# Kernel optimization log

Hardware: AMD Instinct MI355X
Metric: run time of the kernel (lower is better)

Reference implementation:

```python
import jax, jax.numpy as jnp
import numpy as np
import math

B, C_IN, N_SEL, N_DROP, HEADS = 4, 128, 1024, 1024, 4
Q_OUT = K_OUT = V_OUT = 256
N = N_SEL + N_DROP


def setup_inputs() -> dict:
    key = jax.random.key(0)
    ks = jax.random.split(key, 8)
    pcd_up = jax.random.normal(ks[0], (B, C_IN, N), jnp.float32)
    points_select = jax.random.normal(ks[1], (B, C_IN, N_SEL), jnp.float32)
    points_drop = jax.random.normal(ks[2], (B, C_IN, N_DROP), jnp.float32)
    # per-batch permutation of [0, N) split into select/drop halves (collision-free scatter)
    perms = jax.vmap(lambda k: jax.random.permutation(k, N))(jax.random.split(ks[3], B))
    idx_select = perms[:, None, :N_SEL].astype(jnp.int32)
    idx_drop = perms[:, None, N_SEL:].astype(jnp.int32)
    scale = 1.0 / math.sqrt(C_IN)
    Wq = jax.random.normal(ks[4], (Q_OUT, C_IN), jnp.float32) * scale
    Wk = jax.random.normal(ks[5], (K_OUT, C_IN), jnp.float32) * scale
    Wv = jax.random.normal(ks[6], (V_OUT, C_IN), jnp.float32) * scale
    Wskip = jax.random.normal(ks[7], (V_OUT, C_IN), jnp.float32) * scale
    return {"pcd_up": pcd_up, "points_select": points_select, "points_drop": points_drop,
            "idx_select": idx_select, "idx_drop": idx_drop,
            "Wq": Wq, "Wk": Wk, "Wv": Wv, "Wskip": Wskip}


def _concat_by_idx(a, b, idx_a, idx_b):
    # scatter columns of concat([a,b]) to positions given by concat([idx_a, idx_b])
    src = jnp.concatenate([a, b], axis=-1)            # (B, C, N)
    idx = jnp.concatenate([idx_a, idx_b], axis=-1)[:, 0, :]  # (B, N)
    return jax.vmap(lambda s, i: jnp.zeros_like(s).at[:, i].set(s))(src, idx)


def reference(pcd_up, points_select, points_drop, idx_select, idx_drop, Wq, Wk, Wv, Wskip):
    b, _, n = pcd_up.shape
    x = _concat_by_idx(points_select, points_drop, idx_select, idx_drop)  # (B, C_in, N)
    # 1x1 convs (no bias) == channel matmuls, then split heads: (B, H, D, N)
    q = jnp.einsum('oc,bcn->bon', Wq, x).reshape(b, HEADS, Q_OUT // HEADS, n)
    k = jnp.einsum('oc,bcn->bon', Wk, x).reshape(b, HEADS, K_OUT // HEADS, n)
    v = jnp.einsum('oc,bcn->bon', Wv, x).reshape(b, HEADS, V_OUT // HEADS, n)
    energy = jnp.einsum('bhdn,bhdm->bhnm', q, k)      # (B, H, N, N)
    attn = jax.nn.softmax(energy / math.sqrt(Q_OUT // HEADS), axis=-1)
    out = jnp.einsum('bhnm,bhdm->bhnd', attn, v)      # (B, H, N, Dv)
    out = out.transpose(0, 2, 1, 3).reshape(b, n, V_OUT).transpose(0, 2, 1)  # (B, V_out, N)
    skip = jnp.einsum('oc,bcn->bon', Wskip, pcd_up)   # (B, V_out, N)
    return skip + out
```

## Files before the change

kernel.cpp:

```cpp
#include <hip/hip_runtime.h>
#include <hip/hip_bf16.h>
#include <math.h>

#define B_    4
#define C_IN_ 128
#define N_    2048
#define NSEL_ 1024
#define H_    4
#define KS_   2

typedef __bf16 bf16;
typedef __bf16 bf16x2 __attribute__((ext_vector_type(2)));
typedef __bf16 bf16x4 __attribute__((ext_vector_type(4)));
typedef __bf16 bf16x8 __attribute__((ext_vector_type(8)));
typedef float  f32x4  __attribute__((ext_vector_type(4)));

__device__ __forceinline__ void gll16(const void* g, void* l) {
    __builtin_amdgcn_global_load_lds((const __attribute__((address_space(1))) void*)g,
                                     (__attribute__((address_space(3))) void*)l,
                                     16, 0, 0);
}

__device__ __forceinline__ bf16x8 cvt8(float4 a, float4 b) {
    bf16x8 r;
    r[0] = (bf16)a.x; r[1] = (bf16)a.y; r[2] = (bf16)a.z; r[3] = (bf16)a.w;
    r[4] = (bf16)b.x; r[5] = (bf16)b.y; r[6] = (bf16)b.z; r[7] = (bf16)b.w;
    return r;
}

__device__ __forceinline__ float fast_exp2(float x) {
#if __has_builtin(__builtin_amdgcn_exp2f)
    return __builtin_amdgcn_exp2f(x);
#else
    return exp2f(x);
#endif
}

#define XSTR 136

__global__ __launch_bounds__(256) void qkv_mfma_kernel(
    const float* __restrict__ sel, const float* __restrict__ drop,
    const float* __restrict__ Wq, const float* __restrict__ Wk,
    const float* __restrict__ Wv,
    const int* __restrict__ isel, const int* __restrict__ idrp,
    int* __restrict__ inv,
    bf16* __restrict__ qT, bf16* __restrict__ kTt, bf16* __restrict__ vTt)
{
    const int ntile = blockIdx.x;
    const int which = blockIdx.y >> 1;
    const int rh    = blockIdx.y & 1;
    const int b     = blockIdx.z;
    const int tid   = threadIdx.x;
    const int w     = tid >> 6;
    const int lane  = tid & 63;
    const int quad  = lane >> 4;
    const int lc    = lane & 15;
    const int n0    = ntile * 64;

    __shared__ __align__(16) bf16 xT[64 * XSTR];

    if (blockIdx.y == 0 && ntile < 8) {
        int j = ntile * 256 + tid;
        int pos = (j < NSEL_) ? isel[b * NSEL_ + j] : idrp[b * NSEL_ + (j - NSEL_)];
        inv[b * N_ + (pos & (N_ - 1))] = j;
    }

    const float* srcp; int rstride;
    if (ntile < 16) { srcp = sel  + (size_t)b * C_IN_ * NSEL_ + n0;           rstride = NSEL_; }
    else            { srcp = drop + (size_t)b * C_IN_ * NSEL_ + (n0 - NSEL_); rstride = NSEL_; }

    #pragma unroll
    for (int k = 0; k < 4; ++k) {
        int e  = tid + k * 256;
        int cp = e >> 4, nq = e & 15;
        int c0 = cp * 2;
        float4 v0 = *(const float4*)(srcp + (size_t)c0 * rstride + nq * 4);
        float4 v1 = *(const float4*)(srcp + (size_t)(c0 + 1) * rstride + nq * 4);
        int cc = c0 ^ ((nq & 3) << 3);
        float a0[4] = {v0.x, v0.y, v0.z, v0.w};
        float a1[4] = {v1.x, v1.y, v1.z, v1.w};
        #pragma unroll
        for (int i = 0; i < 4; ++i) {
            int n = nq * 4 + i;
            bf16x2 t; t[0] = (bf16)a0[i]; t[1] = (bf16)a1[i];
            *(bf16x2*)&xT[n * XSTR + cc] = t;
        }
    }
    __syncthreads();

    const float* Wx = (which == 0) ? Wq : (which == 1) ? Wk : Wv;
    const int rbase = rh * 128 + w * 32;

    f32x4 acc[8];
    #pragma unroll
    for (int i = 0; i < 8; ++i) acc[i] = (f32x4){0.f, 0.f, 0.f, 0.f};

    #pragma unroll
    for (int kq = 0; kq < 4; ++kq) {
        bf16x8 wf[2], xA[4];
        #pragma unroll
        for (int ot = 0; ot < 2; ++ot) {
            const float* wp = Wx + (size_t)(rbase + ot * 16 + lc) * 128 + kq * 32 + quad * 8;
            float4 u0 = *(const float4*)wp;
            float4 u1 = *(const float4*)(wp + 4);
            wf[ot] = cvt8(u0, u1);
        }
        #pragma unroll
        for (int nt = 0; nt < 4; ++nt) {
            int row = nt * 16 + lc;
            int col = (kq * 32 + quad * 8) ^ (((row >> 2) & 3) << 3);
            xA[nt] = *(const bf16x8*)&xT[row * XSTR + col];
        }
        if (which <= 1) {
            #pragma unroll
            for (int nt = 0; nt < 4; ++nt)
                #pragma unroll
                for (int ot = 0; ot < 2; ++ot)
                    acc[nt * 2 + ot] = __builtin_amdgcn_mfma_f32_16x16x32_bf16(xA[nt], wf[ot], acc[nt * 2 + ot], 0, 0, 0);
        } else {
            #pragma unroll
            for (int ot = 0; ot < 2; ++ot)
                #pragma unroll
                for (int nt = 0; nt < 4; ++nt)
                    acc[ot * 4 + nt] = __builtin_amdgcn_mfma_f32_16x16x32_bf16(wf[ot], xA[nt], acc[ot * 4 + nt], 0, 0, 0);
        }
    }

    if (which <= 1) {
        #pragma unroll
        for (int nt = 0; nt < 4; ++nt) {
            #pragma unroll
            for (int ot = 0; ot < 2; ++ot) {
                #pragma unroll
                for (int r = 0; r < 4; ++r) {
                    int n    = n0 + nt * 16 + quad * 4 + r;
                    int rloc = nt * 16 + quad * 4 + r;
                    int o256 = rbase + ot * 16 + lc;
                    int h = o256 >> 6, d = o256 & 63;
                    float val = acc[nt * 2 + ot][r];
                    if (which == 0)
                        qT[((size_t)(b * H_ + h) * N_ + n) * 64 + d] = (bf16)(val * 0.18033688011f);
                    else
                        kTt[(((size_t)(b * H_ + h) * 32 + ntile) << 12) | (rloc << 6) | (d ^ ((rloc & 7) << 3))] = (bf16)val;
                }
            }
        }
    } else {
        #pragma unroll
        for (int ot = 0; ot < 2; ++ot) {
            #pragma unroll
            for (int r = 0; r < 4; ++r) {
                int o256 = rbase + ot * 16 + quad * 4 + r;
                int h = o256 >> 6, dv = o256 & 63;
                bf16x4 pk;
                #pragma unroll
                for (int nt = 0; nt < 4; ++nt) pk[nt] = (bf16)acc[ot * 4 + nt][r];
                int scol = (lc * 4) ^ ((dv & 7) << 3);
                *(bf16x4*)(vTt + ((((size_t)(b * H_ + h) * 32 + ntile) << 12) | (dv << 6) | scol)) = pk;
            }
        }
    }
}

#define PSTR 72

__global__ __launch_bounds__(256, 2) void attn_kernel(
    const bf16* __restrict__ qT, const bf16* __restrict__ kTt,
    const bf16* __restrict__ vTt, bf16* __restrict__ Opart,
    float* __restrict__ S_ws)
{
    const int id    = blockIdx.x;
    const int bh    = (id & 7) + 8 * ((id >> 3) & 1);
    const int qb    = (id >> 4) & 15;
    const int c     = id >> 8;
    const int b     = bh >> 2;
    const int h     = bh & 3;
    const int tid   = threadIdx.x;
    const int w     = tid >> 6;
    const int lane  = tid & 63;
    const int quad  = lane >> 4;
    const int lc    = lane & 15;
    const int n0    = qb * 128 + w * 32;

    __shared__ __align__(16) bf16 sK[2][64 * 64];
    __shared__ __align__(16) bf16 sV[2][64 * 64];
    __shared__ __align__(16) bf16 p_lds[4 * 16 * PSTR];
    bf16* pw = &p_lds[w * 16 * PSTR];

    const bf16* kbase = kTt + (((size_t)bh * 32 + c * 16) << 12);
    const bf16* vbase = vTt + (((size_t)bh * 32 + c * 16) << 12);

    #pragma unroll
    for (int j = 0; j < 2; ++j) {
        const int sseg = (w * 2 + j) << 9;
        gll16(kbase + sseg + lane * 8, &sK[0][sseg]);
        gll16(vbase + sseg + lane * 8, &sV[0][sseg]);
    }

    bf16x8 aq[2][2];
    #pragma unroll
    for (int t = 0; t < 2; ++t) {
        const bf16* qp = qT + ((size_t)bh * N_ + n0 + t * 16 + lc) * 64 + quad * 8;
        aq[t][0] = *(const bf16x8*)(qp);
        aq[t][1] = *(const bf16x8*)(qp + 32);
    }

    f32x4 accO[2][4];
    #pragma unroll
    for (int t = 0; t < 2; ++t)
        #pragma unroll
        for (int i = 0; i < 4; ++i) accO[t][i] = (f32x4){0.f, 0.f, 0.f, 0.f};
    float psum[2][4] = {{0.f,0.f,0.f,0.f},{0.f,0.f,0.f,0.f}};

    const int rswz = (lc & 7) << 3;

    for (int s = 0; s < 16; ++s) {
        const int buf = s & 1;
        __syncthreads();

        if (s < 15) {
            const bf16* kg = kbase + ((size_t)(s + 1) << 12);
            const bf16* vg = vbase + ((size_t)(s + 1) << 12);
            #pragma unroll
            for (int j = 0; j < 2; ++j) {
                const int sseg = (w * 2 + j) << 9;
                gll16(kg + sseg + lane * 8, &sK[buf ^ 1][sseg]);
                gll16(vg + sseg + lane * 8, &sV[buf ^ 1][sseg]);
            }
        }

        bf16x8 kf[4][2], vf[4][2];
        #pragma unroll
        for (int mt = 0; mt < 4; ++mt) {
            const int rb = (mt * 16 + lc) * 64;
            kf[mt][0] = *(const bf16x8*)&sK[buf][rb + ((quad * 8) ^ rswz)];
            kf[mt][1] = *(const bf16x8*)&sK[buf][rb + ((quad * 8 + 32) ^ rswz)];
            vf[mt][0] = *(const bf16x8*)&sV[buf][rb + ((quad * 8) ^ rswz)];
            vf[mt][1] = *(const bf16x8*)&sV[buf][rb + ((quad * 8 + 32) ^ rswz)];
        }

        #pragma unroll
        for (int t = 0; t < 2; ++t) {
            f32x4 accS[4];
            #pragma unroll
            for (int mt = 0; mt < 4; ++mt) {
                f32x4 z = (f32x4){0.f, 0.f, 0.f, 0.f};
                z = __builtin_amdgcn_mfma_f32_16x16x32_bf16(aq[t][0], kf[mt][0], z, 0, 0, 0);
                z = __builtin_amdgcn_mfma_f32_16x16x32_bf16(aq[t][1], kf[mt][1], z, 0, 0, 0);
                accS[mt] = z;
            }
            #pragma unroll
            for (int r = 0; r < 4; ++r) {
                float sum = 0.f;
                #pragma unroll
                for (int mt = 0; mt < 4; ++mt) {
                    float p = fast_exp2(accS[mt][r]);
                    accS[mt][r] = p;
                    sum += p;
                }
                psum[t][r] += sum;
            }
            #pragma unroll
            for (int r = 0; r < 4; ++r) {
                bf16x4 pk;
                #pragma unroll
                for (int mt = 0; mt < 4; ++mt) pk[mt] = (bf16)accS[mt][r];
                *(bf16x4*)&pw[(quad * 4 + r) * PSTR + lc * 4] = pk;
            }
            bf16x8 ap0 = *(const bf16x8*)(&pw[lc * PSTR + quad * 8]);
            bf16x8 ap1 = *(const bf16x8*)(&pw[lc * PSTR + 32 + quad * 8]);
            #pragma unroll
            for (int dvt = 0; dvt < 4; ++dvt) {
                accO[t][dvt] = __builtin_amdgcn_mfma_f32_16x16x32_bf16(ap0, vf[dvt][0], accO[t][dvt], 0, 0, 0);
                accO[t][dvt] = __builtin_amdgcn_mfma_f32_16x16x32_bf16(ap1, vf[dvt][1], accO[t][dvt], 0, 0, 0);
            }
        }
    }

    #pragma unroll
    for (int t = 0; t < 2; ++t) {
        float inv_[4];
        #pragma unroll
        for (int r = 0; r < 4; ++r) {
            float s = psum[t][r];
            #pragma unroll
            for (int off = 1; off < 16; off <<= 1)
                s += __shfl_xor(s, off, 64);
            inv_[r] = 1.f / s;
            int n = n0 + t * 16 + quad * 4 + r;
            if (lc == 0)
                S_ws[((size_t)(c * B_ + b) * H_ + h) * N_ + n] = s;
        }
        #pragma unroll
        for (int r = 0; r < 4; ++r) {
            int n = n0 + t * 16 + quad * 4 + r;
            #pragma unroll
            for (int dvt = 0; dvt < 4; ++dvt) {
                int o = h * 64 + dvt * 16 + lc;
                Opart[((size_t)(c * B_ + b) * N_ + n) * 256 + o] = (bf16)(accO[t][dvt][r] * inv_[r]);
            }
        }
    }
}

__global__ __launch_bounds__(256) void scatter_kernel(
    const bf16* __restrict__ Opart, const float* __restrict__ S_ws,
    const int* __restrict__ inv, const float* __restrict__ pcd,
    const float* __restrict__ Ws, float* __restrict__ out)
{
    const int ptile = blockIdx.x;
    const int og    = blockIdx.y;
    const int b     = blockIdx.z;
    const int tid   = threadIdx.x;
    const int w     = tid >> 6;
    const int lane  = tid & 63;
    const int quad  = lane >> 4;
    const int lc    = lane & 15;
    const int p0    = ptile * 64;

    __shared__ __align__(16) bf16 xT[64 * XSTR];
    __shared__ __align__(16) bf16 lds[64 * 72];

    const int row0 = tid >> 3, seg = tid & 7, row1 = row0 + 32;
    int j0 = inv[b * N_ + p0 + row0] & (N_ - 1);
    int j1 = inv[b * N_ + p0 + row1] & (N_ - 1);
    float sv0[KS_], sv1[KS_];
    bf16x8 g0[KS_], g1[KS_];
    #pragma unroll
    for (int cc = 0; cc < KS_; ++cc) {
        g0[cc] = *(const bf16x8*)(Opart + (((size_t)(cc * B_ + b) * N_ + j0) << 8) + og * 64 + seg * 8);
        g1[cc] = *(const bf16x8*)(Opart + (((size_t)(cc * B_ + b) * N_ + j1) << 8) + og * 64 + seg * 8);
        sv0[cc] = S_ws[((size_t)(cc * B_ + b) * H_ + og) * N_ + j0];
        sv1[cc] = S_ws[((size_t)(cc * B_ + b) * H_ + og) * N_ + j1];
    }

    const float* srcp = pcd + (size_t)b * C_IN_ * N_ + p0;
    #pragma unroll
    for (int k = 0; k < 4; ++k) {
        int e  = tid + k * 256;
        int cp = e >> 4, nq = e & 15;
        int c0 = cp * 2;
        float4 v0 = *(const float4*)(srcp + (size_t)c0 * N_ + nq * 4);
        float4 v1 = *(const float4*)(srcp + (size_t)(c0 + 1) * N_ + nq * 4);
        int cc = c0 ^ ((nq & 3) << 3);
        float a0[4] = {v0.x, v0.y, v0.z, v0.w};
        float a1[4] = {v1.x, v1.y, v1.z, v1.w};
        #pragma unroll
        for (int i = 0; i < 4; ++i) {
            int n = nq * 4 + i;
            bf16x2 t; t[0] = (bf16)a0[i]; t[1] = (bf16)a1[i];
            *(bf16x2*)&xT[n * XSTR + cc] = t;
        }
    }
    __syncthreads();

    f32x4 acc[4];
    #pragma unroll
    for (int i = 0; i < 4; ++i) acc[i] = (f32x4){0.f, 0.f, 0.f, 0.f};
    #pragma unroll
    for (int kq = 0; kq < 4; ++kq) {
        const float* wp = Ws + (size_t)(og * 64 + w * 16 + lc) * 128 + kq * 32 + quad * 8;
        float4 u0 = *(const float4*)wp;
        float4 u1 = *(const float4*)(wp + 4);
        bf16x8 A = cvt8(u0, u1);
        #pragma unroll
        for (int nt = 0; nt < 4; ++nt) {
            int row = nt * 16 + lc;
            int col = (kq * 32 + quad * 8) ^ (((row >> 2) & 3) << 3);
            bf16x8 Bf = *(const bf16x8*)&xT[row * XSTR + col];
            acc[nt] = __builtin_amdgcn_mfma_f32_16x16x32_bf16(A, Bf, acc[nt], 0, 0, 0);
        }
    }

    {
        float d0 = 0.f, d1 = 0.f;
        #pragma unroll
        for (int cc = 0; cc < KS_; ++cc) { d0 += sv0[cc]; d1 += sv1[cc]; }
        float id0 = 1.f / d0, id1 = 1.f / d1;
        float a8[8], b8[8];
        #pragma unroll
        for (int i = 0; i < 8; ++i) { a8[i] = 0.f; b8[i] = 0.f; }
        #pragma unroll
        for (int cc = 0; cc < KS_; ++cc) {
            float w0 = sv0[cc] * id0, w1 = sv1[cc] * id1;
            #pragma unroll
            for (int i = 0; i < 8; ++i) {
                a8[i] += w0 * (float)g0[cc][i];
                b8[i] += w1 * (float)g1[cc][i];
            }
        }
        bf16x8 o8, p8;
        #pragma unroll
        for (int i = 0; i < 8; ++i) { o8[i] = (bf16)a8[i]; p8[i] = (bf16)b8[i]; }
        *(bf16x8*)&lds[row0 * 72 + seg * 8] = o8;
        *(bf16x8*)&lds[row1 * 72 + seg * 8] = p8;
    }
    __syncthreads();

    #pragma unroll
    for (int nt = 0; nt < 4; ++nt) {
        #pragma unroll
        for (int r = 0; r < 4; ++r) {
            int o_loc = w * 16 + quad * 4 + r;
            int p     = nt * 16 + lc;
            float attn = (float)lds[p * 72 + o_loc];
            out[((size_t)b * 256 + og * 64 + o_loc) * N_ + p0 + p] = acc[nt][r] + attn;
        }
    }
}

extern "C" void kernel_launch(void* const* d_in, const int* in_sizes, int n_in,
                              void* d_out, int out_size, void* d_ws, size_t ws_size,
                              hipStream_t stream) {
    const float* pcd  = (const float*)d_in[0];
    const float* sel  = (const float*)d_in[1];
    const float* drop = (const float*)d_in[2];
    const int*   isel = (const int*)d_in[3];
    const int*   idrp = (const int*)d_in[4];
    const float* Wq   = (const float*)d_in[5];
    const float* Wk   = (const float*)d_in[6];
    const float* Wv   = (const float*)d_in[7];
    const float* Ws   = (const float*)d_in[8];
    float* out = (float*)d_out;

    const size_t MB = 1024 * 1024;
    char*  ws    = (char*)d_ws;
    bf16*  qT    = (bf16*)(ws);
    bf16*  kTt   = (bf16*)(ws + 4 * MB);
    bf16*  vTt   = (bf16*)(ws + 8 * MB);
    bf16*  Opart = (bf16*)(ws + 12 * MB);
    float* S_ws  = (float*)(ws + 20 * MB);
    int*   inv   = (int*)(ws + 20 * MB + 256 * 1024);

    qkv_mfma_kernel<<<dim3(32, 6, B_), 256, 0, stream>>>(sel, drop, Wq, Wk, Wv,
                                                         isel, idrp, inv,
                                                         qT, kTt, vTt);
    attn_kernel<<<dim3(16 * 16 * KS_), 256, 0, stream>>>(qT, kTt, vTt, Opart, S_ws);
    scatter_kernel<<<dim3(32, 4, B_), 256, 0, stream>>>(Opart, S_ws, inv, pcd, Ws, out);
}
```

Before: 121.7 us.

## Enlarge attention query tile, raise key split, prebake bf16 weights in prep kernel

Each attention block now handles 256 queries (64 per wave) against 8 key chunks instead of 128 queries against 16 chunks. The key split factor goes from 2 to 4, so the grid stays at 512 blocks while each K/V tile loaded into LDS is reused by twice as many queries. A new prep kernel converts all four weight matrices to bf16 once and builds the inverse index, so the QKV and skip kernels no longer convert fp32 weights per block. The costs are an extra kernel launch, more accumulator registers per wave in the attention kernel (occupancy risk), and more partial results for the scatter kernel to combine.

```diff
diff --git a/kernel.cpp b/kernel.cpp
--- a/kernel.cpp
+++ b/kernel.cpp
@@ -7,7 +7,7 @@
 #define N_    2048
 #define NSEL_ 1024
 #define H_    4
-#define KS_   2
+#define KS_   4
 
 typedef __bf16 bf16;
 typedef __bf16 bf16x2 __attribute__((ext_vector_type(2)));
@@ -19,13 +19,6 @@
     __builtin_amdgcn_global_load_lds((const __attribute__((address_space(1))) void*)g,
                                      (__attribute__((address_space(3))) void*)l,
                                      16, 0, 0);
-}
-
-__device__ __forceinline__ bf16x8 cvt8(float4 a, float4 b) {
-    bf16x8 r;
-    r[0] = (bf16)a.x; r[1] = (bf16)a.y; r[2] = (bf16)a.z; r[3] = (bf16)a.w;
-    r[4] = (bf16)b.x; r[5] = (bf16)b.y; r[6] = (bf16)b.z; r[7] = (bf16)b.w;
-    return r;
 }
 
 __device__ __forceinline__ float fast_exp2(float x) {
@@ -36,14 +29,34 @@
 #endif
 }
 
+__global__ __launch_bounds__(256) void prep_kernel(
+    const int* __restrict__ isel, const int* __restrict__ idrp,
+    const float* __restrict__ Wq, const float* __restrict__ Wk,
+    const float* __restrict__ Wv, const float* __restrict__ Ws,
+    int* __restrict__ inv, bf16* __restrict__ Wbf)
+{
+    const int blk = blockIdx.x;
+    if (blk < 128) {
+        int e = blk * 256 + threadIdx.x;
+        int which = e >> 13, idx = e & 8191;
+        const float* Wx = (which == 0) ? Wq : (which == 1) ? Wk
+                        : (which == 2) ? Wv : Ws;
+        float4 v = *(const float4*)(Wx + (size_t)idx * 4);
+        bf16x4 o; o[0] = (bf16)v.x; o[1] = (bf16)v.y; o[2] = (bf16)v.z; o[3] = (bf16)v.w;
+        *(bf16x4*)(Wbf + (size_t)which * 32768 + (size_t)idx * 4) = o;
+    } else {
+        int g = (blk - 128) * 256 + threadIdx.x;
+        int b = g >> 11, j = g & (N_ - 1);
+        int pos = (j < NSEL_) ? isel[b * NSEL_ + j] : idrp[b * NSEL_ + (j - NSEL_)];
+        inv[b * N_ + (pos & (N_ - 1))] = j;
+    }
+}
+
 #define XSTR 136
 
 __global__ __launch_bounds__(256) void qkv_mfma_kernel(
     const float* __restrict__ sel, const float* __restrict__ drop,
-    const float* __restrict__ Wq, const float* __restrict__ Wk,
-    const float* __restrict__ Wv,
-    const int* __restrict__ isel, const int* __restrict__ idrp,
-    int* __restrict__ inv,
+    const bf16* __restrict__ Wbf,
     bf16* __restrict__ qT, bf16* __restrict__ kTt, bf16* __restrict__ vTt)
 {
     const int ntile = blockIdx.x;
@@ -59,12 +72,6 @@
 
     __shared__ __align__(16) bf16 xT[64 * XSTR];
 
-    if (blockIdx.y == 0 && ntile < 8) {
-        int j = ntile * 256 + tid;
-        int pos = (j < NSEL_) ? isel[b * NSEL_ + j] : idrp[b * NSEL_ + (j - NSEL_)];
-        inv[b * N_ + (pos & (N_ - 1))] = j;
-    }
-
     const float* srcp; int rstride;
     if (ntile < 16) { srcp = sel  + (size_t)b * C_IN_ * NSEL_ + n0;           rstride = NSEL_; }
     else            { srcp = drop + (size_t)b * C_IN_ * NSEL_ + (n0 - NSEL_); rstride = NSEL_; }
@@ -88,7 +95,7 @@
     }
     __syncthreads();
 
-    const float* Wx = (which == 0) ? Wq : (which == 1) ? Wk : Wv;
+    const bf16* wbase = Wbf + (size_t)which * 256 * 128;
     const int rbase = rh * 128 + w * 32;
 
     f32x4 acc[8];
@@ -99,12 +106,8 @@
     for (int kq = 0; kq < 4; ++kq) {
         bf16x8 wf[2], xA[4];
         #pragma unroll
-        for (int ot = 0; ot < 2; ++ot) {
-            const float* wp = Wx + (size_t)(rbase + ot * 16 + lc) * 128 + kq * 32 + quad * 8;
-            float4 u0 = *(const float4*)wp;
-            float4 u1 = *(const float4*)(wp + 4);
-            wf[ot] = cvt8(u0, u1);
-        }
+        for (int ot = 0; ot < 2; ++ot)
+            wf[ot] = *(const bf16x8*)(wbase + (size_t)(rbase + ot * 16 + lc) * 128 + kq * 32 + quad * 8);
         #pragma unroll
         for (int nt = 0; nt < 4; ++nt) {
             int row = nt * 16 + lc;
@@ -171,8 +174,8 @@
 {
     const int id    = blockIdx.x;
     const int bh    = (id & 7) + 8 * ((id >> 3) & 1);
-    const int qb    = (id >> 4) & 15;
-    const int c     = id >> 8;
+    const int qb    = (id >> 4) & 7;
+    const int c     = id >> 7;
     const int b     = bh >> 2;
     const int h     = bh & 3;
     const int tid   = threadIdx.x;
@@ -180,15 +183,15 @@
     const int lane  = tid & 63;
     const int quad  = lane >> 4;
     const int lc    = lane & 15;
-    const int n0    = qb * 128 + w * 32;
+    const int n0    = qb * 256 + w * 64;
 
     __shared__ __align__(16) bf16 sK[2][64 * 64];
     __shared__ __align__(16) bf16 sV[2][64 * 64];
     __shared__ __align__(16) bf16 p_lds[4 * 16 * PSTR];
     bf16* pw = &p_lds[w * 16 * PSTR];
 
-    const bf16* kbase = kTt + (((size_t)bh * 32 + c * 16) << 12);
-    const bf16* vbase = vTt + (((size_t)bh * 32 + c * 16) << 12);
+    const bf16* kbase = kTt + (((size_t)bh * 32 + c * 8) << 12);
+    const bf16* vbase = vTt + (((size_t)bh * 32 + c * 8) << 12);
 
     #pragma unroll
     for (int j = 0; j < 2; ++j) {
@@ -197,28 +200,29 @@
         gll16(vbase + sseg + lane * 8, &sV[0][sseg]);
     }
 
-    bf16x8 aq[2][2];
-    #pragma unroll
-    for (int t = 0; t < 2; ++t) {
+    bf16x8 aq[4][2];
+    #pragma unroll
+    for (int t = 0; t < 4; ++t) {
         const bf16* qp = qT + ((size_t)bh * N_ + n0 + t * 16 + lc) * 64 + quad * 8;
         aq[t][0] = *(const bf16x8*)(qp);
         aq[t][1] = *(const bf16x8*)(qp + 32);
     }
 
-    f32x4 accO[2][4];
-    #pragma unroll
-    for (int t = 0; t < 2; ++t)
+    f32x4 accO[4][4];
+    #pragma unroll
+    for (int t = 0; t < 4; ++t)
         #pragma unroll
         for (int i = 0; i < 4; ++i) accO[t][i] = (f32x4){0.f, 0.f, 0.f, 0.f};
-    float psum[2][4] = {{0.f,0.f,0.f,0.f},{0.f,0.f,0.f,0.f}};
+    float psum[4][4] = {{0.f,0.f,0.f,0.f},{0.f,0.f,0.f,0.f},
+                        {0.f,0.f,0.f,0.f},{0.f,0.f,0.f,0.f}};
 
     const int rswz = (lc & 7) << 3;
 
-    for (int s = 0; s < 16; ++s) {
+    for (int s = 0; s < 8; ++s) {
         const int buf = s & 1;
         __syncthreads();
 
-        if (s < 15) {
+        if (s < 7) {
             const bf16* kg = kbase + ((size_t)(s + 1) << 12);
             const bf16* vg = vbase + ((size_t)(s + 1) << 12);
             #pragma unroll
@@ -240,7 +244,7 @@
         }
 
         #pragma unroll
-        for (int t = 0; t < 2; ++t) {
+        for (int t = 0; t < 4; ++t) {
             f32x4 accS[4];
             #pragma unroll
             for (int mt = 0; mt < 4; ++mt) {
@@ -278,7 +282,7 @@
     }
 
     #pragma unroll
-    for (int t = 0; t < 2; ++t) {
+    for (int t = 0; t < 4; ++t) {
         float inv_[4];
         #pragma unroll
         for (int r = 0; r < 4; ++r) {
@@ -306,7 +310,7 @@
 __global__ __launch_bounds__(256) void scatter_kernel(
     const bf16* __restrict__ Opart, const float* __restrict__ S_ws,
     const int* __restrict__ inv, const float* __restrict__ pcd,
-    const float* __restrict__ Ws, float* __restrict__ out)
+    const bf16* __restrict__ Wbf, float* __restrict__ out)
 {
     const int ptile = blockIdx.x;
     const int og    = blockIdx.y;
@@ -354,15 +358,13 @@
     }
     __syncthreads();
 
+    const bf16* wbase = Wbf + (size_t)3 * 256 * 128 + (size_t)(og * 64 + w * 16) * 128;
     f32x4 acc[4];
     #pragma unroll
     for (int i = 0; i < 4; ++i) acc[i] = (f32x4){0.f, 0.f, 0.f, 0.f};
     #pragma unroll
     for (int kq = 0; kq < 4; ++kq) {
-        const float* wp = Ws + (size_t)(og * 64 + w * 16 + lc) * 128 + kq * 32 + quad * 8;
-        float4 u0 = *(const float4*)wp;
-        float4 u1 = *(const float4*)(wp + 4);
-        bf16x8 A = cvt8(u0, u1);
+        bf16x8 A = *(const bf16x8*)(wbase + (size_t)lc * 128 + kq * 32 + quad * 8);
         #pragma unroll
         for (int nt = 0; nt < 4; ++nt) {
             int row = nt * 16 + lc;
@@ -429,12 +431,13 @@
     bf16*  kTt   = (bf16*)(ws + 4 * MB);
     bf16*  vTt   = (bf16*)(ws + 8 * MB);
     bf16*  Opart = (bf16*)(ws + 12 * MB);
-    float* S_ws  = (float*)(ws + 20 * MB);
-    int*   inv   = (int*)(ws + 20 * MB + 256 * 1024);
-
-    qkv_mfma_kernel<<<dim3(32, 6, B_), 256, 0, stream>>>(sel, drop, Wq, Wk, Wv,
-                                                         isel, idrp, inv,
+    float* S_ws  = (float*)(ws + 28 * MB);
+    bf16*  Wbf   = (bf16*)(ws + 28 * MB + 512 * 1024);
+    int*   inv   = (int*)(ws + 28 * MB + 768 * 1024);
+
+    prep_kernel<<<dim3(160), 256, 0, stream>>>(isel, idrp, Wq, Wk, Wv, Ws, inv, Wbf);
+    qkv_mfma_kernel<<<dim3(32, 6, B_), 256, 0, stream>>>(sel, drop, Wbf,
                                                          qT, kTt, vTt);
-    attn_kernel<<<dim3(16 * 16 * KS_), 256, 0, stream>>>(qT, kTt, vTt, Opart, S_ws);
-    scatter_kernel<<<dim3(32, 4, B_), 256, 0, stream>>>(Opart, S_ws, inv, pcd, Ws, out);
-}
+    attn_kernel<<<dim3(16 * 8 * KS_), 256, 0, stream>>>(qT, kTt, vTt, Opart, S_ws);
+    scatter_kernel<<<dim3(32, 4, B_), 256, 0, stream>>>(Opart, S_ws, inv, pcd, Wbf, out);
+}
```

Result: faster. 117.8 us (median of 2 runs) (-3.2%).
